# Performance work log

Measured on AMD Instinct MI355X. Metric: run time of the kernel, lower is better.

Reference implementation:

```python
import jax, jax.numpy as jnp
import numpy as np

N = 100000
F = 256
H = 128
C = 64
E = 1600000

def spmm(rows, cols, vals, h):
    # sparse [N,N] @ dense [N,D] via gather + segment-sum
    return jax.ops.segment_sum(vals[:, None] * h[cols], rows, num_segments=N)

def graph_conv(x, W, rows, cols, vals, b=None):
    # GraphConv: support = x @ W; out = adj @ support (+ bias)
    out = spmm(rows, cols, vals, x @ W)
    if b is not None:
        out = out + b
    return out

def setup_inputs() -> dict:
    key = jax.random.key(0)
    ks = jax.random.split(key, 20)
    d = {}
    d['x'] = jax.random.normal(ks[0], (N, F), dtype=jnp.float32)
    for i, name in enumerate(['mid', 'low', 'high']):
        d[name + '_rows'] = jax.random.randint(ks[1 + 3 * i], (E,), 0, N, dtype=jnp.int64 if jax.config.jax_enable_x64 else jnp.int32)
        d[name + '_cols'] = jax.random.randint(ks[2 + 3 * i], (E,), 0, N, dtype=jnp.int64 if jax.config.jax_enable_x64 else jnp.int32)
        d[name + '_vals'] = jax.random.uniform(ks[3 + 3 * i], (E,), dtype=jnp.float32) * 0.1
    s = lambda k, a, b_: jax.random.normal(k, (a, b_), dtype=jnp.float32) * (1.0 / np.sqrt(a))
    d['W_hid'] = s(ks[10], F, H)          # hidden_layers[0], no bias
    d['W_out'] = s(ks[11], H, C)          # out_layer
    d['b_out'] = jnp.zeros((C,), jnp.float32)
    d['W_low'] = s(ks[12], F, H)          # addHid_layer, no bias
    d['W_low_out'] = s(ks[13], H, C)      # addOut_layer
    d['b_low_out'] = jnp.zeros((C,), jnp.float32)
    d['W_high'] = s(ks[14], F, H)         # addHid_layer_HIGH, no bias
    d['W_high_out'] = s(ks[15], H, C)     # addOut_layer_HIGH
    d['b_high_out'] = jnp.zeros((C,), jnp.float32)
    d['gate2'] = jnp.array([0.5], jnp.float32)
    return d

def reference(x, mid_rows, mid_cols, mid_vals, low_rows, low_cols, low_vals,
              high_rows, high_cols, high_vals, W_hid, W_out, b_out,
              W_low, W_low_out, b_low_out, W_high, W_high_out, b_high_out, gate2):
    # dropout is identity at inference
    h = jax.nn.relu(graph_conv(x, W_hid, mid_rows, mid_cols, mid_vals))
    h = graph_conv(h, W_out, mid_rows, mid_cols, mid_vals, b_out)
    x2 = jax.nn.relu(graph_conv(x, W_low, low_rows, low_cols, low_vals))
    xh = jax.nn.relu(graph_conv(x, W_high, high_rows, high_cols, high_vals))
    x2 = graph_conv(x2, W_low_out, low_rows, low_cols, low_vals, b_low_out)
    xh = graph_conv(xh, W_high_out, high_rows, high_cols, high_vals, b_high_out)
    x_final = gate2 * h + (1.0 - gate2) * (x2 + xh)
    return jax.nn.log_softmax(x_final, axis=-1)
```

## Files before the change

### kernel.cpp

```cpp
#include <hip/hip_runtime.h>
#include <math.h>

#define NNODES 100000
#define NEDGES 1600000
#define FEAT 256
#define HID 128
#define NCLS 64
#define RPB 512
#define NBG 196
#define NB3 (3 * NBG)
#define CAP 8832
#define SC_CHUNK 8192
#define SC_THREADS 1024

typedef __attribute__((ext_vector_type(8))) short bf16x8;
typedef __attribute__((ext_vector_type(4))) float f32x4;
typedef __attribute__((ext_vector_type(2))) float f32x2;

__device__ __forceinline__ unsigned short f2bf(float f) {
  union { float f; unsigned int i; } c; c.f = f;
  unsigned int u = c.i;
  return (unsigned short)((u + 0x7fffu + ((u >> 16) & 1u)) >> 16);
}

__device__ __forceinline__ void fma8(const uint4 u, const f32x2 vv, f32x2* a) {
  f32x2 p0, p1, p2, p3;
  p0.x = __uint_as_float(u.x << 16); p0.y = __uint_as_float(u.x & 0xffff0000u);
  p1.x = __uint_as_float(u.y << 16); p1.y = __uint_as_float(u.y & 0xffff0000u);
  p2.x = __uint_as_float(u.z << 16); p2.y = __uint_as_float(u.z & 0xffff0000u);
  p3.x = __uint_as_float(u.w << 16); p3.y = __uint_as_float(u.w & 0xffff0000u);
  a[0] += p0 * vv; a[1] += p1 * vv; a[2] += p2 * vv; a[3] += p3 * vv;
}

__global__ __launch_bounds__(256) void k_bhist(const int* __restrict__ r0,
                                               const int* __restrict__ r1,
                                               const int* __restrict__ r2,
                                               int* __restrict__ bhist) {
  __shared__ int h[NBG];
  int g = blockIdx.y;
  const int* rr = (g == 0) ? r0 : (g == 1 ? r1 : r2);
  int tid = threadIdx.x;
  for (int i = tid; i < NBG; i += 256) h[i] = 0;
  __syncthreads();
  int base = blockIdx.x * 4096;
#pragma unroll
  for (int k = 0; k < 16; k++) {
    int e = base + k * 256 + tid;
    if (e < NEDGES) atomicAdd(&h[rr[e] >> 9], 1);
  }
  __syncthreads();
  for (int i = tid; i < NBG; i += 256)
    if (h[i]) atomicAdd(&bhist[g * NBG + i], h[i]);
}

__global__ __launch_bounds__(1024) void k_bscan(const int* __restrict__ bhist,
                                                int* __restrict__ boff) {
  __shared__ int sd[2][1024];
  int tid = threadIdx.x;
  int v = (tid < NB3) ? bhist[tid] : 0;
  sd[0][tid] = v;
  __syncthreads();
  int cur = 0;
  for (int off = 1; off < 1024; off <<= 1) {
    int nv = sd[cur][tid];
    if (tid >= off) nv += sd[cur][tid - off];
    sd[cur ^ 1][tid] = nv;
    __syncthreads();
    cur ^= 1;
  }
  int incl = sd[cur][tid];
  if (tid < NB3) boff[tid] = incl - v;
  if (tid == NB3 - 1) boff[NB3] = incl;
}

__global__ __launch_bounds__(SC_THREADS) void k_bucket_scatter(
    const int* __restrict__ r0, const int* __restrict__ r1, const int* __restrict__ r2,
    const int* __restrict__ c0, const int* __restrict__ c1, const int* __restrict__ c2,
    const float* __restrict__ v0, const float* __restrict__ v1, const float* __restrict__ v2,
    int* __restrict__ gcur, int2* __restrict__ edges) {
  __shared__ int2 stage[SC_CHUNK];
  __shared__ unsigned char bid[SC_CHUNK];
  __shared__ int hist[NBG];
  __shared__ int lbase[NBG];
  __shared__ int gstart[NBG];
  __shared__ int cur[NBG];
  __shared__ int sd[2][256];
  int g = blockIdx.y;
  const int*   rr = (g == 0) ? r0 : (g == 1 ? r1 : r2);
  const int*   cc = (g == 0) ? c0 : (g == 1 ? c1 : c2);
  const float* vv = (g == 0) ? v0 : (g == 1 ? v1 : v2);
  int tid = threadIdx.x;
  int base = blockIdx.x * SC_CHUNK;
  int cnt_blk = NEDGES - base;
  if (cnt_blk > SC_CHUNK) cnt_blk = SC_CHUNK;

  for (int i = tid; i < NBG; i += SC_THREADS) hist[i] = 0;
  __syncthreads();

  int rowv[SC_CHUNK / SC_THREADS];
  int colv[SC_CHUNK / SC_THREADS];
  float valv[SC_CHUNK / SC_THREADS];
#pragma unroll
  for (int k = 0; k < SC_CHUNK / SC_THREADS; k++) {
    int e = base + k * SC_THREADS + tid;
    bool ok = e < NEDGES;
    rowv[k] = ok ? rr[e] : -1;
    colv[k] = ok ? cc[e] : 0;
    valv[k] = ok ? vv[e] : 0.f;
    if (ok) atomicAdd(&hist[rowv[k] >> 9], 1);
  }
  __syncthreads();

  if (tid < 256) sd[0][tid] = (tid < NBG) ? hist[tid] : 0;
  __syncthreads();
  int c = 0;
  for (int off = 1; off < 256; off <<= 1) {
    if (tid < 256) {
      int nv = sd[c][tid];
      if (tid >= off) nv += sd[c][tid - off];
      sd[c ^ 1][tid] = nv;
    }
    __syncthreads();
    c ^= 1;
  }
  if (tid < NBG) {
    int cn = hist[tid];
    int excl = sd[c][tid] - cn;
    lbase[tid] = excl;
    cur[tid] = excl;
    gstart[tid] = cn ? atomicAdd(&gcur[g * NBG + tid], cn) : 0;
  }
  __syncthreads();

#pragma unroll
  for (int k = 0; k < SC_CHUNK / SC_THREADS; k++) {
    if (rowv[k] >= 0) {
      int b = rowv[k] >> 9;
      int p = atomicAdd(&cur[b], 1);
      stage[p] = make_int2(((rowv[k] & (RPB - 1)) << 17) | colv[k], __float_as_int(valv[k]));
      bid[p] = (unsigned char)b;
    }
  }
  __syncthreads();

  for (int i = tid; i < cnt_blk; i += SC_THREADS) {
    int b = bid[i];
    int dst = gstart[b] + (i - lbase[b]);
    edges[dst] = stage[i];
  }
}

__global__ __launch_bounds__(512) void k_bucket_sort(const int* __restrict__ boff,
                                                     int2* __restrict__ edges,
                                                     int* __restrict__ row_ptr_all) {
  __shared__ int2 stage[CAP];
  __shared__ int hist[RPB];
  __shared__ int sd[2][RPB];
  __shared__ int cur[RPB];
  int g = blockIdx.y, b = blockIdx.x;
  int tid = threadIdx.x;
  int idx = g * NBG + b;
  int base = boff[idx];
  int count = boff[idx + 1] - base;
  if (count > CAP) count = CAP;
  hist[tid] = 0;
  __syncthreads();

  const int KSL = (CAP + 511) / 512;
  int2 ev[KSL];
#pragma unroll
  for (int k = 0; k < KSL; k++) {
    int i = tid + k * 512;
    if (i < count) {
      ev[k] = edges[base + i];
      atomicAdd(&hist[ev[k].x >> 17], 1);
    }
  }
  __syncthreads();

  int v = hist[tid];
  sd[0][tid] = v;
  __syncthreads();
  int c2 = 0;
  for (int off = 1; off < 512; off <<= 1) {
    int nv = sd[c2][tid];
    if (tid >= off) nv += sd[c2][tid - off];
    sd[c2 ^ 1][tid] = nv;
    __syncthreads();
    c2 ^= 1;
  }
  int excl = sd[c2][tid] - v;
  int row = b * RPB + tid;
  if (row <= NNODES) row_ptr_all[g * (NNODES + 1) + row] = base + excl;
  cur[tid] = excl;
  __syncthreads();

#pragma unroll
  for (int k = 0; k < KSL; k++) {
    int i = tid + k * 512;
    if (i < count) {
      int lr = ev[k].x >> 17;
      int p = atomicAdd(&cur[lr], 1);
      stage[p] = make_int2(ev[k].x & 0x1FFFF, ev[k].y);
    }
  }
  __syncthreads();

  for (int i = tid; i < count; i += 512) edges[base + i] = stage[i];
}

__global__ __launch_bounds__(256) void k_convert_bf16(const float* __restrict__ src,
                                                      unsigned short* __restrict__ dst,
                                                      int n4) {
  int i = blockIdx.x * blockDim.x + threadIdx.x;
  if (i < n4) {
    float4 v = ((const float4*)src)[i];
    ushort4 o;
    o.x = f2bf(v.x); o.y = f2bf(v.y); o.z = f2bf(v.z); o.w = f2bf(v.w);
    ((ushort4*)dst)[i] = o;
  }
}

__global__ __launch_bounds__(256) void k_transpose3(const float* __restrict__ s0,
                                                    const float* __restrict__ s1,
                                                    const float* __restrict__ s2,
                                                    unsigned short* __restrict__ d0,
                                                    unsigned short* __restrict__ d1,
                                                    unsigned short* __restrict__ d2,
                                                    int K, int N) {
  int g = blockIdx.y;
  const float* src = (g == 0) ? s0 : (g == 1 ? s1 : s2);
  unsigned short* dst = (g == 0) ? d0 : (g == 1 ? d1 : d2);
  int idx = blockIdx.x * 256 + threadIdx.x;
  if (idx < K * N) {
    int k = idx / N, n = idx % N;
    dst[(size_t)n * K + k] = f2bf(src[idx]);
  }
}

__global__ __launch_bounds__(256) void k_gemm1_b(const unsigned short* __restrict__ A,
                                                 const unsigned short* __restrict__ WtA,
                                                 unsigned short* __restrict__ C3, int M) {
  int bxy = blockIdx.x;
  int g = bxy % 3;
  int bx = bxy / 3;
  const unsigned short* Wt = WtA + (size_t)g * HID * FEAT;
  unsigned short* C = C3 + (size_t)g * M * HID;
  int tid = threadIdx.x;
  int wave = tid >> 6, lane = tid & 63;
  int quad = lane >> 4, r = lane & 15;
  int m0 = bx * 128 + wave * 32;
  int ra0 = m0 + r;      if (ra0 >= M) ra0 = 0;
  int ra1 = m0 + 16 + r; if (ra1 >= M) ra1 = 0;
  const unsigned short* pa0 = A + (size_t)ra0 * FEAT + quad * 8;
  const unsigned short* pa1 = A + (size_t)ra1 * FEAT + quad * 8;
  f32x4 acc[2][8];
#pragma unroll
  for (int i = 0; i < 2; i++)
#pragma unroll
    for (int j = 0; j < 8; j++) acc[i][j] = (f32x4){0.f, 0.f, 0.f, 0.f};
  for (int k0 = 0; k0 < FEAT; k0 += 32) {
    bf16x8 a0 = *(const bf16x8*)(pa0 + k0);
    bf16x8 a1 = *(const bf16x8*)(pa1 + k0);
#pragma unroll
    for (int nt = 0; nt < 8; nt++) {
      bf16x8 b = *(const bf16x8*)(Wt + (size_t)(nt * 16 + r) * FEAT + k0 + quad * 8);
      acc[0][nt] = __builtin_amdgcn_mfma_f32_16x16x32_bf16(a0, b, acc[0][nt], 0, 0, 0);
      acc[1][nt] = __builtin_amdgcn_mfma_f32_16x16x32_bf16(a1, b, acc[1][nt], 0, 0, 0);
    }
  }
#pragma unroll
  for (int t = 0; t < 2; t++)
#pragma unroll
    for (int reg = 0; reg < 4; reg++) {
      int row = m0 + t * 16 + quad * 4 + reg;
      if (row < M) {
#pragma unroll
        for (int nt = 0; nt < 8; nt++)
          C[(size_t)row * HID + nt * 16 + r] = f2bf(acc[t][nt][reg]);
      }
    }
}

__global__ __launch_bounds__(256) void k_gemm2_b(const unsigned short* __restrict__ A3,
                                                 const unsigned short* __restrict__ WtA,
                                                 unsigned short* __restrict__ C3, int M) {
  int g = blockIdx.y;
  const unsigned short* A = A3 + (size_t)g * M * HID;
  const unsigned short* Wt = WtA + (size_t)g * NCLS * HID;
  unsigned short* C = C3 + (size_t)g * M * NCLS;
  int tid = threadIdx.x;
  int wave = tid >> 6, lane = tid & 63;
  int quad = lane >> 4, r = lane & 15;
  int m0 = blockIdx.x * 128 + wave * 32;
  int ra0 = m0 + r;      if (ra0 >= M) ra0 = 0;
  int ra1 = m0 + 16 + r; if (ra1 >= M) ra1 = 0;
  const unsigned short* pa0 = A + (size_t)ra0 * HID + quad * 8;
  const unsigned short* pa1 = A + (size_t)ra1 * HID + quad * 8;
  f32x4 acc[2][4];
#pragma unroll
  for (int i = 0; i < 2; i++)
#pragma unroll
    for (int j = 0; j < 4; j++) acc[i][j] = (f32x4){0.f, 0.f, 0.f, 0.f};
  for (int k0 = 0; k0 < HID; k0 += 32) {
    bf16x8 a0 = *(const bf16x8*)(pa0 + k0);
    bf16x8 a1 = *(const bf16x8*)(pa1 + k0);
#pragma unroll
    for (int nt = 0; nt < 4; nt++) {
      bf16x8 b = *(const bf16x8*)(Wt + (size_t)(nt * 16 + r) * HID + k0 + quad * 8);
      acc[0][nt] = __builtin_amdgcn_mfma_f32_16x16x32_bf16(a0, b, acc[0][nt], 0, 0, 0);
      acc[1][nt] = __builtin_amdgcn_mfma_f32_16x16x32_bf16(a1, b, acc[1][nt], 0, 0, 0);
    }
  }
#pragma unroll
  for (int t = 0; t < 2; t++)
#pragma unroll
    for (int reg = 0; reg < 4; reg++) {
      int row = m0 + t * 16 + quad * 4 + reg;
      if (row < M) {
#pragma unroll
        for (int nt = 0; nt < 4; nt++)
          C[(size_t)row * NCLS + nt * 16 + r] = f2bf(acc[t][nt][reg]);
      }
    }
}

__global__ __launch_bounds__(256) void k_spmm128_b(const int* __restrict__ rp_all,
                                                   const int2* __restrict__ edges,
                                                   const unsigned short* __restrict__ dense3,
                                                   unsigned short* __restrict__ out3, int n) {
  int g = blockIdx.y;
  const int* rp = rp_all + (size_t)g * (NNODES + 1);
  const unsigned short* dense = dense3 + (size_t)g * NNODES * HID;
  unsigned short* out = out3 + (size_t)g * NNODES * HID;
  int w = (blockIdx.x * blockDim.x + threadIdx.x) >> 6;
  int lane = threadIdx.x & 63;
  if (w >= n) return;
  int grp = lane >> 4;
  int sub = lane & 15;
  int s = rp[w], e = rp[w + 1];
  f32x2 a0[4], a1[4];
#pragma unroll
  for (int q = 0; q < 4; q++) { a0[q] = (f32x2){0.f, 0.f}; a1[q] = (f32x2){0.f, 0.f}; }
  for (int j = s; j < e; j += 8) {
    int e0 = j + grp, e1 = j + 4 + grp;
    bool k0 = e0 < e, k1 = e1 < e;
    int2 d0 = edges[k0 ? e0 : s];
    int2 d1 = edges[k1 ? e1 : s];
    uint4 u0 = *(const uint4*)(dense + (size_t)d0.x * HID + sub * 8);
    uint4 u1 = *(const uint4*)(dense + (size_t)d1.x * HID + sub * 8);
    float f0 = k0 ? __int_as_float(d0.y) : 0.f;
    float f1 = k1 ? __int_as_float(d1.y) : 0.f;
    f32x2 v0; v0.x = f0; v0.y = f0;
    f32x2 v1; v1.x = f1; v1.y = f1;
    fma8(u0, v0, a0);
    fma8(u1, v1, a1);
  }
  unsigned int pk[4];
#pragma unroll
  for (int q = 0; q < 4; q++) {
    float lo = a0[q].x + a1[q].x;
    float hi = a0[q].y + a1[q].y;
    lo += __shfl_xor(lo, 32, 64); lo += __shfl_xor(lo, 16, 64);
    hi += __shfl_xor(hi, 32, 64); hi += __shfl_xor(hi, 16, 64);
    lo = fmaxf(lo, 0.f); hi = fmaxf(hi, 0.f);
    pk[q] = (unsigned int)f2bf(lo) | ((unsigned int)f2bf(hi) << 16);
  }
  if (lane < 16) {
    uint4 o; o.x = pk[0]; o.y = pk[1]; o.z = pk[2]; o.w = pk[3];
    *(uint4*)(out + (size_t)w * HID + sub * 8) = o;
  }
}

__global__ __launch_bounds__(256) void k_spmm64_final(const int* __restrict__ rp_all,
                                                      const int2* __restrict__ edges,
                                                      const unsigned short* __restrict__ dense3,
                                                      const float* __restrict__ b0p,
                                                      const float* __restrict__ b1p,
                                                      const float* __restrict__ b2p,
                                                      const float* __restrict__ gate,
                                                      float* __restrict__ outp, int n) {
  int w = (blockIdx.x * blockDim.x + threadIdx.x) >> 6;
  int lane = threadIdx.x & 63;
  if (w >= n) return;
  int grp = lane >> 3;
  int sub = lane & 7;
  int s[3], e[3];
#pragma unroll
  for (int g = 0; g < 3; g++) {
    s[g] = __builtin_amdgcn_readfirstlane(rp_all[(size_t)g * (NNODES + 1) + w]);
    e[g] = __builtin_amdgcn_readfirstlane(rp_all[(size_t)g * (NNODES + 1) + w + 1]);
  }
  int nit = 0;
#pragma unroll
  for (int g = 0; g < 3; g++) {
    int t = (e[g] - s[g] + 7) >> 3;
    nit = (t > nit) ? t : nit;
  }
  f32x2 ac0[4], ac1[4], ac2[4];
#pragma unroll
  for (int q = 0; q < 4; q++) {
    ac0[q] = (f32x2){0.f, 0.f}; ac1[q] = (f32x2){0.f, 0.f}; ac2[q] = (f32x2){0.f, 0.f};
  }
  const unsigned short* d0b = dense3;
  const unsigned short* d1b = dense3 + (size_t)NNODES * NCLS;
  const unsigned short* d2b = dense3 + (size_t)2 * NNODES * NCLS;
  for (int it = 0; it < nit; it++) {
    int j0 = s[0] + it * 8 + grp, j1 = s[1] + it * 8 + grp, j2 = s[2] + it * 8 + grp;
    bool k0 = j0 < e[0], k1 = j1 < e[1], k2 = j2 < e[2];
    int2 d0 = edges[k0 ? j0 : s[0]];
    int2 d1 = edges[k1 ? j1 : s[1]];
    int2 d2 = edges[k2 ? j2 : s[2]];
    uint4 u0 = *(const uint4*)(d0b + (size_t)d0.x * NCLS + sub * 8);
    uint4 u1 = *(const uint4*)(d1b + (size_t)d1.x * NCLS + sub * 8);
    uint4 u2 = *(const uint4*)(d2b + (size_t)d2.x * NCLS + sub * 8);
    float f0 = k0 ? __int_as_float(d0.y) : 0.f;
    float f1 = k1 ? __int_as_float(d1.y) : 0.f;
    float f2 = k2 ? __int_as_float(d2.y) : 0.f;
    f32x2 v0; v0.x = f0; v0.y = f0;
    f32x2 v1; v1.x = f1; v1.y = f1;
    f32x2 v2; v2.x = f2; v2.y = f2;
    fma8(u0, v0, ac0);
    fma8(u1, v1, ac1);
    fma8(u2, v2, ac2);
  }
  float gv = gate[0];
  float omg = 1.0f - gv;
  float tot[8];
  {
    float4 x0 = *(const float4*)(b0p + sub * 8), x1 = *(const float4*)(b0p + sub * 8 + 4);
    float4 y0 = *(const float4*)(b1p + sub * 8), y1 = *(const float4*)(b1p + sub * 8 + 4);
    float4 z0 = *(const float4*)(b2p + sub * 8), z1 = *(const float4*)(b2p + sub * 8 + 4);
    tot[0] = gv * x0.x + omg * (y0.x + z0.x); tot[1] = gv * x0.y + omg * (y0.y + z0.y);
    tot[2] = gv * x0.z + omg * (y0.z + z0.z); tot[3] = gv * x0.w + omg * (y0.w + z0.w);
    tot[4] = gv * x1.x + omg * (y1.x + z1.x); tot[5] = gv * x1.y + omg * (y1.y + z1.y);
    tot[6] = gv * x1.z + omg * (y1.z + z1.z); tot[7] = gv * x1.w + omg * (y1.w + z1.w);
  }
#pragma unroll
  for (int q = 0; q < 4; q++) {
    float lo = gv * ac0[q].x + omg * (ac1[q].x + ac2[q].x);
    float hi = gv * ac0[q].y + omg * (ac1[q].y + ac2[q].y);
    lo += __shfl_xor(lo, 32, 64); lo += __shfl_xor(lo, 16, 64); lo += __shfl_xor(lo, 8, 64);
    hi += __shfl_xor(hi, 32, 64); hi += __shfl_xor(hi, 16, 64); hi += __shfl_xor(hi, 8, 64);
    tot[2 * q] += lo;
    tot[2 * q + 1] += hi;
  }
  float m = tot[0];
#pragma unroll
  for (int i = 1; i < 8; i++) m = fmaxf(m, tot[i]);
  m = fmaxf(m, __shfl_xor(m, 1, 64));
  m = fmaxf(m, __shfl_xor(m, 2, 64));
  m = fmaxf(m, __shfl_xor(m, 4, 64));
  float sum = 0.f;
#pragma unroll
  for (int i = 0; i < 8; i++) sum += expf(tot[i] - m);
  sum += __shfl_xor(sum, 1, 64);
  sum += __shfl_xor(sum, 2, 64);
  sum += __shfl_xor(sum, 4, 64);
  float ls = m + logf(sum);
  if (grp == 0) {
    size_t o = (size_t)w * NCLS + sub * 8;
    *(float4*)(outp + o)     = make_float4(tot[0] - ls, tot[1] - ls, tot[2] - ls, tot[3] - ls);
    *(float4*)(outp + o + 4) = make_float4(tot[4] - ls, tot[5] - ls, tot[6] - ls, tot[7] - ls);
  }
}

extern "C" void kernel_launch(void* const* d_in, const int* in_sizes, int n_in,
                              void* d_out, int out_size, void* d_ws, size_t ws_size,
                              hipStream_t stream) {
  (void)in_sizes; (void)n_in; (void)out_size; (void)ws_size;
  const float* x = (const float*)d_in[0];
  const int*   rows[3]   = {(const int*)d_in[1], (const int*)d_in[4], (const int*)d_in[7]};
  const int*   colsIn[3] = {(const int*)d_in[2], (const int*)d_in[5], (const int*)d_in[8]};
  const float* valsIn[3] = {(const float*)d_in[3], (const float*)d_in[6], (const float*)d_in[9]};
  const float* Whid[3] = {(const float*)d_in[10], (const float*)d_in[13], (const float*)d_in[16]};
  const float* Wout[3] = {(const float*)d_in[11], (const float*)d_in[14], (const float*)d_in[17]};
  const float* bout[3] = {(const float*)d_in[12], (const float*)d_in[15], (const float*)d_in[18]};
  const float* gate = (const float*)d_in[19];
  float* out = (float*)d_out;

  const int N = NNODES, E = NEDGES;
  size_t off = 0;
  auto ws = [&](size_t bytes) {
    void* p = (char*)d_ws + off;
    off += (bytes + 255) & ~(size_t)255;
    return p;
  };
  unsigned short* R1 = (unsigned short*)ws((size_t)3 * N * HID * 2);
  unsigned short* x_bf = R1;
  unsigned short* h13  = R1;
  unsigned short* hsup3 = (unsigned short*)ws((size_t)3 * N * HID * 2);
  unsigned short* Wt1a = (unsigned short*)ws((size_t)3 * HID * FEAT * 2);
  unsigned short* Wt2a = (unsigned short*)ws((size_t)3 * NCLS * HID * 2);
  int2* edges   = (int2*)ws(((size_t)3 * E + 64) * 8);
  int*  rp_all  = (int*) ws((size_t)3 * (N + 1) * 4);
  int*  bhist   = (int*) ws(NB3 * 4);
  int*  boff    = (int*) ws((NB3 + 1) * 4);
  int*  gcur    = (int*) ws(NB3 * 4);

  dim3 b256(256);
  dim3 gRows3((N + 3) / 4, 3);
  int nbGemm = (N + 127) / 128;

  k_convert_bf16<<<(N * FEAT / 4 + 255) / 256, b256, 0, stream>>>(x, x_bf, N * FEAT / 4);
  k_transpose3<<<dim3((FEAT * HID + 255) / 256, 3), b256, 0, stream>>>(
      Whid[0], Whid[1], Whid[2], Wt1a, Wt1a + (size_t)HID * FEAT, Wt1a + (size_t)2 * HID * FEAT,
      FEAT, HID);
  k_transpose3<<<dim3((HID * NCLS + 255) / 256, 3), b256, 0, stream>>>(
      Wout[0], Wout[1], Wout[2], Wt2a, Wt2a + (size_t)NCLS * HID, Wt2a + (size_t)2 * NCLS * HID,
      HID, NCLS);

  hipMemsetAsync(bhist, 0, NB3 * 4, stream);
  k_bhist<<<dim3((E + 4095) / 4096, 3), b256, 0, stream>>>(rows[0], rows[1], rows[2], bhist);
  k_bscan<<<1, 1024, 0, stream>>>(bhist, boff);
  hipMemcpyAsync(gcur, boff, NB3 * 4, hipMemcpyDeviceToDevice, stream);
  k_bucket_scatter<<<dim3((E + SC_CHUNK - 1) / SC_CHUNK, 3), dim3(SC_THREADS), 0, stream>>>(
      rows[0], rows[1], rows[2], colsIn[0], colsIn[1], colsIn[2],
      valsIn[0], valsIn[1], valsIn[2], gcur, edges);
  k_bucket_sort<<<dim3(NBG, 3), 512, 0, stream>>>(boff, edges, rp_all);

  k_gemm1_b<<<dim3(3 * nbGemm), b256, 0, stream>>>(x_bf, Wt1a, hsup3, N);
  k_spmm128_b<<<gRows3, b256, 0, stream>>>(rp_all, edges, hsup3, h13, N);
  k_gemm2_b<<<dim3(nbGemm, 3), b256, 0, stream>>>(h13, Wt2a, hsup3, N);
  k_spmm64_final<<<dim3((N + 3) / 4), b256, 0, stream>>>(
      rp_all, edges, hsup3, bout[0], bout[1], bout[2], gate, out, N);
}
```

Before: 697.5 us.

## Merge prep kernels into one launch, fold gcur copy, prefetch edges in spmm64

Combines the x bf16 conversion, both weight transposes and the bucket histogram into a single k_prep launch that dispatches on block index, which removes several kernel launches. The scan kernel now writes gcur directly, replacing a device-to-device memcpy. The final SpMM loop software-prefetches the next iteration's edge entries so the index load overlaps the gather of dense rows. The cost is a larger heterogeneous kernel, more register pressure in the SpMM loop, and an extra, possibly out-of-range-clamped, edge load after the last iteration.

```diff
diff --git a/kernel.cpp b/kernel.cpp
--- a/kernel.cpp
+++ b/kernel.cpp
@@ -32,29 +32,72 @@
   a[0] += p0 * vv; a[1] += p1 * vv; a[2] += p2 * vv; a[3] += p3 * vv;
 }
 
-__global__ __launch_bounds__(256) void k_bhist(const int* __restrict__ r0,
-                                               const int* __restrict__ r1,
-                                               const int* __restrict__ r2,
-                                               int* __restrict__ bhist) {
+#define NB_CONV 25000
+#define NB_T1 128
+#define NB_T2 32
+#define NB_BH 391
+#define PREP_BLOCKS (NB_CONV + 3 * NB_T1 + 3 * NB_T2 + 3 * NB_BH)
+
+__global__ __launch_bounds__(256) void k_prep(
+    const float* __restrict__ x, unsigned short* __restrict__ x_bf,
+    const float* __restrict__ W10, const float* __restrict__ W11, const float* __restrict__ W12,
+    unsigned short* __restrict__ Wt1a,
+    const float* __restrict__ W20, const float* __restrict__ W21, const float* __restrict__ W22,
+    unsigned short* __restrict__ Wt2a,
+    const int* __restrict__ r0, const int* __restrict__ r1, const int* __restrict__ r2,
+    int* __restrict__ bhist) {
   __shared__ int h[NBG];
-  int g = blockIdx.y;
-  const int* rr = (g == 0) ? r0 : (g == 1 ? r1 : r2);
+  int b = blockIdx.x;
   int tid = threadIdx.x;
-  for (int i = tid; i < NBG; i += 256) h[i] = 0;
-  __syncthreads();
-  int base = blockIdx.x * 4096;
-#pragma unroll
-  for (int k = 0; k < 16; k++) {
-    int e = base + k * 256 + tid;
-    if (e < NEDGES) atomicAdd(&h[rr[e] >> 9], 1);
-  }
-  __syncthreads();
-  for (int i = tid; i < NBG; i += 256)
-    if (h[i]) atomicAdd(&bhist[g * NBG + i], h[i]);
+  if (b < NB_CONV) {
+    int i = b * 256 + tid;
+    float4 v = ((const float4*)x)[i];
+    ushort4 o;
+    o.x = f2bf(v.x); o.y = f2bf(v.y); o.z = f2bf(v.z); o.w = f2bf(v.w);
+    ((ushort4*)x_bf)[i] = o;
+    return;
+  }
+  b -= NB_CONV;
+  if (b < 3 * NB_T1) {
+    int g = b / NB_T1, bx = b % NB_T1;
+    const float* src = (g == 0) ? W10 : (g == 1 ? W11 : W12);
+    unsigned short* dst = Wt1a + (size_t)g * HID * FEAT;
+    int idx = bx * 256 + tid;
+    int k = idx / HID, n = idx % HID;
+    dst[(size_t)n * FEAT + k] = f2bf(src[idx]);
+    return;
+  }
+  b -= 3 * NB_T1;
+  if (b < 3 * NB_T2) {
+    int g = b / NB_T2, bx = b % NB_T2;
+    const float* src = (g == 0) ? W20 : (g == 1 ? W21 : W22);
+    unsigned short* dst = Wt2a + (size_t)g * NCLS * HID;
+    int idx = bx * 256 + tid;
+    int k = idx / NCLS, n = idx % NCLS;
+    dst[(size_t)n * HID + k] = f2bf(src[idx]);
+    return;
+  }
+  b -= 3 * NB_T2;
+  {
+    int g = b / NB_BH, bx = b % NB_BH;
+    const int* rr = (g == 0) ? r0 : (g == 1 ? r1 : r2);
+    for (int i = tid; i < NBG; i += 256) h[i] = 0;
+    __syncthreads();
+    int base = bx * 4096;
+#pragma unroll
+    for (int k = 0; k < 16; k++) {
+      int e = base + k * 256 + tid;
+      if (e < NEDGES) atomicAdd(&h[rr[e] >> 9], 1);
+    }
+    __syncthreads();
+    for (int i = tid; i < NBG; i += 256)
+      if (h[i]) atomicAdd(&bhist[g * NBG + i], h[i]);
+  }
 }
 
 __global__ __launch_bounds__(1024) void k_bscan(const int* __restrict__ bhist,
-                                                int* __restrict__ boff) {
+                                                int* __restrict__ boff,
+                                                int* __restrict__ gcur) {
   __shared__ int sd[2][1024];
   int tid = threadIdx.x;
   int v = (tid < NB3) ? bhist[tid] : 0;
@@ -69,7 +112,7 @@
     cur ^= 1;
   }
   int incl = sd[cur][tid];
-  if (tid < NB3) boff[tid] = incl - v;
+  if (tid < NB3) { boff[tid] = incl - v; gcur[tid] = incl - v; }
   if (tid == NB3 - 1) boff[NB3] = incl;
 }
 
@@ -209,35 +252,6 @@
   for (int i = tid; i < count; i += 512) edges[base + i] = stage[i];
 }
 
-__global__ __launch_bounds__(256) void k_convert_bf16(const float* __restrict__ src,
-                                                      unsigned short* __restrict__ dst,
-                                                      int n4) {
-  int i = blockIdx.x * blockDim.x + threadIdx.x;
-  if (i < n4) {
-    float4 v = ((const float4*)src)[i];
-    ushort4 o;
-    o.x = f2bf(v.x); o.y = f2bf(v.y); o.z = f2bf(v.z); o.w = f2bf(v.w);
-    ((ushort4*)dst)[i] = o;
-  }
-}
-
-__global__ __launch_bounds__(256) void k_transpose3(const float* __restrict__ s0,
-                                                    const float* __restrict__ s1,
-                                                    const float* __restrict__ s2,
-                                                    unsigned short* __restrict__ d0,
-                                                    unsigned short* __restrict__ d1,
-                                                    unsigned short* __restrict__ d2,
-                                                    int K, int N) {
-  int g = blockIdx.y;
-  const float* src = (g == 0) ? s0 : (g == 1 ? s1 : s2);
-  unsigned short* dst = (g == 0) ? d0 : (g == 1 ? d1 : d2);
-  int idx = blockIdx.x * 256 + threadIdx.x;
-  if (idx < K * N) {
-    int k = idx / N, n = idx % N;
-    dst[(size_t)n * K + k] = f2bf(src[idx]);
-  }
-}
-
 __global__ __launch_bounds__(256) void k_gemm1_b(const unsigned short* __restrict__ A,
                                                  const unsigned short* __restrict__ WtA,
                                                  unsigned short* __restrict__ C3, int M) {
@@ -405,15 +419,21 @@
   const unsigned short* d0b = dense3;
   const unsigned short* d1b = dense3 + (size_t)NNODES * NCLS;
   const unsigned short* d2b = dense3 + (size_t)2 * NNODES * NCLS;
+  int j0 = s[0] + grp, j1 = s[1] + grp, j2 = s[2] + grp;
+  bool k0 = j0 < e[0], k1 = j1 < e[1], k2 = j2 < e[2];
+  int2 d0 = edges[k0 ? j0 : s[0]];
+  int2 d1 = edges[k1 ? j1 : s[1]];
+  int2 d2 = edges[k2 ? j2 : s[2]];
   for (int it = 0; it < nit; it++) {
-    int j0 = s[0] + it * 8 + grp, j1 = s[1] + it * 8 + grp, j2 = s[2] + it * 8 + grp;
-    bool k0 = j0 < e[0], k1 = j1 < e[1], k2 = j2 < e[2];
-    int2 d0 = edges[k0 ? j0 : s[0]];
-    int2 d1 = edges[k1 ? j1 : s[1]];
-    int2 d2 = edges[k2 ? j2 : s[2]];
     uint4 u0 = *(const uint4*)(d0b + (size_t)d0.x * NCLS + sub * 8);
     uint4 u1 = *(const uint4*)(d1b + (size_t)d1.x * NCLS + sub * 8);
     uint4 u2 = *(const uint4*)(d2b + (size_t)d2.x * NCLS + sub * 8);
+    int m0i = s[0] + (it + 1) * 8 + grp, m1i = s[1] + (it + 1) * 8 + grp,
+        m2i = s[2] + (it + 1) * 8 + grp;
+    bool kn0 = m0i < e[0], kn1 = m1i < e[1], kn2 = m2i < e[2];
+    int2 dn0 = edges[kn0 ? m0i : s[0]];
+    int2 dn1 = edges[kn1 ? m1i : s[1]];
+    int2 dn2 = edges[kn2 ? m2i : s[2]];
     float f0 = k0 ? __int_as_float(d0.y) : 0.f;
     float f1 = k1 ? __int_as_float(d1.y) : 0.f;
     float f2 = k2 ? __int_as_float(d2.y) : 0.f;
@@ -423,6 +443,8 @@
     fma8(u0, v0, ac0);
     fma8(u1, v1, ac1);
     fma8(u2, v2, ac2);
+    d0 = dn0; d1 = dn1; d2 = dn2;
+    k0 = kn0; k1 = kn1; k2 = kn2;
   }
   float gv = gate[0];
   float omg = 1.0f - gv;
@@ -502,18 +524,12 @@
   dim3 gRows3((N + 3) / 4, 3);
   int nbGemm = (N + 127) / 128;
 
-  k_convert_bf16<<<(N * FEAT / 4 + 255) / 256, b256, 0, stream>>>(x, x_bf, N * FEAT / 4);
-  k_transpose3<<<dim3((FEAT * HID + 255) / 256, 3), b256, 0, stream>>>(
-      Whid[0], Whid[1], Whid[2], Wt1a, Wt1a + (size_t)HID * FEAT, Wt1a + (size_t)2 * HID * FEAT,
-      FEAT, HID);
-  k_transpose3<<<dim3((HID * NCLS + 255) / 256, 3), b256, 0, stream>>>(
-      Wout[0], Wout[1], Wout[2], Wt2a, Wt2a + (size_t)NCLS * HID, Wt2a + (size_t)2 * NCLS * HID,
-      HID, NCLS);
-
   hipMemsetAsync(bhist, 0, NB3 * 4, stream);
-  k_bhist<<<dim3((E + 4095) / 4096, 3), b256, 0, stream>>>(rows[0], rows[1], rows[2], bhist);
-  k_bscan<<<1, 1024, 0, stream>>>(bhist, boff);
-  hipMemcpyAsync(gcur, boff, NB3 * 4, hipMemcpyDeviceToDevice, stream);
+  k_prep<<<dim3(PREP_BLOCKS), b256, 0, stream>>>(
+      x, x_bf, Whid[0], Whid[1], Whid[2], Wt1a,
+      Wout[0], Wout[1], Wout[2], Wt2a,
+      rows[0], rows[1], rows[2], bhist);
+  k_bscan<<<1, 1024, 0, stream>>>(bhist, boff, gcur);
   k_bucket_scatter<<<dim3((E + SC_CHUNK - 1) / SC_CHUNK, 3), dim3(SC_THREADS), 0, stream>>>(
       rows[0], rows[1], rows[2], colsIn[0], colsIn[1], colsIn[2],
       valsIn[0], valsIn[1], valsIn[2], gcur, edges);
```

New measurement: 690.4 us. About the same (-1.0%).
